# Kernel optimization log

Measured on AMD Instinct MI355X. Metric: run time of the kernel, lower is better.

The kernel has to match this reference:

```python
import jax, jax.numpy as jnp
import numpy as np
from jax.scipy.special import logsumexp

GROUP_LEN = 8
LABEL_SMOOTHING = 0.1
LOSS_TYPES = ("part_slice", "whole_slice", "part_block", "whole_block")
GN, D = 8192, 128


def setup_inputs() -> dict:
    key = jax.random.key(0)
    k1, k2 = jax.random.split(key)
    return {
        "image_features1": jax.random.normal(k1, (GN, D), dtype=jnp.float32),
        "image_features2": jax.random.normal(k2, (GN, D), dtype=jnp.float32),
        "logit_scale": jnp.float32(1.0 / 0.07),
    }


def _group_losses(S, G, N, eps):
    """Vectorized equivalents of the four Python-loop losses on an [GN,GN] logit matrix."""
    GN_ = G * N
    S4 = S.reshape(G, N, G, N)                      # [g, n, g2, n2]
    idx = jnp.arange(G)
    diag_blocks = S4[idx, :, idx, :]                # [G, N, N] (same-group blocks)

    # row-wise quantities
    row_lse = logsumexp(S, axis=1).reshape(G, N)    # [G, N]
    row_sum = S.sum(axis=1).reshape(G, N)           # [G, N]
    pos_sum = diag_blocks.sum(axis=-1)              # [G, N] sum over same-group cols

    # part_slice: mean_i (1-eps)(lse_i - pos_sum_i) + eps/(GN)(lse_i - row_sum_i)
    part_slice = jnp.mean((1.0 - eps) * (row_lse - pos_sum)
                          + (eps / GN_) * (row_lse - row_sum))

    # whole_slice: pos vector is row * y_i -> same-group entries plus (GN-N) zeros,
    # so lse(pos) = logaddexp(lse(diag entries), log(GN - N)) (exp(0)=1 per zero).
    diag_row_lse = logsumexp(diag_blocks, axis=-1)  # [G, N]
    pos_lse = jnp.logaddexp(diag_row_lse, jnp.log(jnp.float32(GN_ - N)))
    blk_row_lse = logsumexp(S4, axis=3)             # [G, N, G] per-row per-block lse
    ws_smooth = (row_lse[:, :, None] - blk_row_lse).sum(axis=-1)  # [G, N]
    whole_slice = jnp.mean((1.0 - eps) * (row_lse - pos_lse) + (eps / G) * ws_smooth)

    # group-level quantities
    grp_lse = logsumexp(S4, axis=(1, 2, 3))         # [G] lse over group's full row band
    grp_sum = S4.sum(axis=(1, 2, 3))                # [G]
    diag_sum = diag_blocks.sum(axis=(1, 2))         # [G]

    # part_block
    part_block = jnp.mean((1.0 - eps) * (grp_lse - diag_sum / (N * N))
                          + eps * (grp_lse - grp_sum / (G * N * N)))

    # whole_block
    blk_lse = logsumexp(S4, axis=(1, 3))            # [G, G] per block lse
    diag_blk_lse = blk_lse[idx, idx]                # [G]
    wb_smooth = (grp_lse[:, None] - blk_lse).sum(axis=-1)  # [G]
    whole_block = jnp.mean((1.0 - eps) * (grp_lse - diag_blk_lse) + (eps / G) * wb_smooth)

    return {"part_slice": part_slice, "whole_slice": whole_slice,
            "part_block": part_block, "whole_block": whole_block}


def reference(image_features1, image_features2, logit_scale):
    f1 = image_features1 / jnp.linalg.norm(image_features1, axis=-1, keepdims=True)
    f2 = image_features2 / jnp.linalg.norm(image_features2, axis=-1, keepdims=True)
    GN_, _ = f1.shape
    N = GROUP_LEN
    G = GN_ // N
    S1 = logit_scale * (f1 @ f2.T)                  # logits_per_image1 [GN, GN]
    S2 = S1.T                                       # logits_per_image2
    eps = LABEL_SMOOTHING
    l1 = _group_losses(S1, G, N, eps)
    l2 = _group_losses(S2, G, N, eps)
    loss = jnp.float32(0.0)
    for lt in LOSS_TYPES:
        loss = loss + 0.5 * (l1[lt] + l2[lt])
    return loss / len(LOSS_TYPES)
```

## Files before the change

kernel.cpp:

```cpp
#include <hip/hip_runtime.h>
#include <math.h>

typedef __attribute__((ext_vector_type(8))) short bf16x8;
typedef __attribute__((ext_vector_type(4))) float f32x4;
typedef unsigned short ushort_t;

#define GN 8192
#define NGRP 1024
#define DDIM 128
#define NCH 16
#define LOG2E 1.4426950408889634f
#define LN2 0.6931471805599453f

#if __has_builtin(__builtin_amdgcn_exp2f)
#define EXP2F(x) __builtin_amdgcn_exp2f(x)
#else
#define EXP2F(x) exp2f(x)
#endif
#if __has_builtin(__builtin_amdgcn_logf)
#define LOG2FAST(x) __builtin_amdgcn_logf(x)
#else
#define LOG2FAST(x) log2f(x)
#endif

#define ROWST 0
#define GRPB  (ROWST + GN*NCH*2)
#define DT    (GRPB + NGRP*NCH)
#define DU8   (DT + 2*GN)
#define GSUM  (DU8 + NGRP)
#define CSUMP (GSUM + 2*NGRP*DDIM)
#define COLP  (CSUMP + 2*32*DDIM)
#define GRP2P (COLP + 128*GN*2)
#define FIN2  (GRP2P + 128*NGRP)
#define SB2   (FIN2 + GN*2)
#define PART  (SB2 + NGRP)

__device__ __forceinline__ ushort_t f2bf(float x) {
  unsigned u = __float_as_uint(x);
  unsigned r = (u + 0x7fffu + ((u >> 16) & 1u)) >> 16;
  return (ushort_t)r;
}
__device__ __forceinline__ float bf2f(unsigned h) {
  return __uint_as_float(h << 16);
}

__device__ __forceinline__ float dpp_shr1_add(float v) {
  int s = __builtin_amdgcn_update_dpp(0, __float_as_int(v), 0x111, 0xF, 0xF, true);
  return v + __int_as_float(s);
}
__device__ __forceinline__ float dpp_shr2_add(float v) {
  int s = __builtin_amdgcn_update_dpp(0, __float_as_int(v), 0x112, 0xF, 0xF, true);
  return v + __int_as_float(s);
}
__device__ __forceinline__ float dpp_shr4_add(float v) {
  int s = __builtin_amdgcn_update_dpp(0, __float_as_int(v), 0x114, 0xF, 0xF, true);
  return v + __int_as_float(s);
}
__device__ __forceinline__ float dpp_ror8_add(float v) {
  int s = __builtin_amdgcn_update_dpp(0, __float_as_int(v), 0x128, 0xF, 0xF, true);
  return v + __int_as_float(s);
}

__global__ __launch_bounds__(256) void normg_kernel(
    const float* __restrict__ f1, const float* __restrict__ f2,
    const float* __restrict__ scp, ushort_t* __restrict__ wsu,
    float* __restrict__ wf) {
  const int b = blockIdx.x;
  const int m = b >> 10;
  const int g = b & 1023;
  const int t = threadIdx.x;
  const int r = t >> 5;
  const int c4 = t & 31;
  const float* __restrict__ f = m ? f2 : f1;
  const float fac0 = m ? 1.0f : (scp[0] * LOG2E);

  const float4 v = ((const float4*)(f + ((size_t)(g * 8 + r)) * DDIM))[c4];
  float ss = v.x * v.x + v.y * v.y + v.z * v.z + v.w * v.w;
  #pragma unroll
  for (int d = 1; d < 32; d <<= 1) ss += __shfl_xor(ss, d);
  const float inv = fac0 / sqrtf(ss);

  ushort4 o;
  o.x = f2bf(v.x * inv); o.y = f2bf(v.y * inv);
  o.z = f2bf(v.z * inv); o.w = f2bf(v.w * inv);
  ((ushort4*)(wsu + (size_t)m * GN * DDIM + (size_t)(g * 8 + r) * DDIM))[c4] = o;

  __shared__ float lds[8][DDIM];
  lds[r][c4 * 4 + 0] = bf2f(o.x);
  lds[r][c4 * 4 + 1] = bf2f(o.y);
  lds[r][c4 * 4 + 2] = bf2f(o.z);
  lds[r][c4 * 4 + 3] = bf2f(o.w);
  __syncthreads();
  if (t < DDIM) {
    float s = 0.f;
    #pragma unroll
    for (int j = 0; j < 8; ++j) s += lds[j][t];
    wf[GSUM + ((size_t)m * NGRP + g) * DDIM + t] = s;
  }
}

__global__ __launch_bounds__(128) void csum_kernel(float* __restrict__ wf) {
  const int b = blockIdx.x;
  const int m = b >> 5;
  const int seg = b & 31;
  const int k = threadIdx.x;
  const float* gp = wf + GSUM + ((size_t)m * NGRP + seg * 32) * DDIM + k;
  float s = 0.f;
  #pragma unroll 8
  for (int g = 0; g < 32; ++g) s += gp[(size_t)g * DDIM];
  wf[CSUMP + ((size_t)m * 32 + seg) * DDIM + k] = s;
}

__global__ __launch_bounds__(256, 4) void gemm_stats(
    const ushort_t* __restrict__ wsu, const float* __restrict__ scp,
    float* __restrict__ wf) {
  const int idx = blockIdx.x;
  const int rowblk = idx >> 4;
  const int chunk = idx & 15;
  const int t = threadIdx.x;
  const int w = t >> 6;
  const int l = t & 63;
  const int li = l & 15;
  const int q = l >> 4;
  const float C = scp[0];
  const float nC2 = -C * LOG2E;

  const ushort_t* A = wsu;
  const ushort_t* B = wsu + (size_t)GN * DDIM;
  const int row0 = rowblk * 64;

  __shared__ ushort_t As[64 * 128];
  {
    const int arow = t >> 2;
    const int aq = t & 3;
    const ushort_t* Agp = A + (size_t)(row0 + arow) * DDIM + aq * 32;
    #pragma unroll
    for (int j = 0; j < 4; ++j) {
      const int swz = (aq * 4 + j) ^ (arow & 15);
      *(uint4*)(As + arow * 128 + swz * 8) = *(const uint4*)(const void*)(Agp + j * 8);
    }
  }
  __syncthreads();

  float esum[4] = {0.f, 0.f, 0.f, 0.f};
  float sbl[4]  = {0.f, 0.f, 0.f, 0.f};
  float sBr[4]  = {0.f, 0.f, 0.f, 0.f};

  const ushort_t* Bp = B + ((size_t)(chunk * 512 + w * 16) + li) * DDIM + q * 8;
  const bool hasdia = (chunk == (row0 >> 9));
  const int idiag = (row0 & 511) >> 6;
  const f32x4 cinit = {nC2, nC2, nC2, nC2};

  #pragma unroll 1
  for (int i = 0; i < 8; ++i) {
    const ushort_t* Bi = Bp + (size_t)i * (64 * DDIM);
    bf16x8 bc[4];
    #pragma unroll
    for (int ks = 0; ks < 4; ++ks)
      bc[ks] = *(const bf16x8*)(const void*)(Bi + ks * 32);

    f32x4 acc[4];
    #pragma unroll
    for (int s = 0; s < 4; ++s) acc[s] = cinit;
    #pragma unroll
    for (int ks = 0; ks < 4; ++ks) {
      int co = (((ks * 4 + q) ^ li) * 8);
      asm volatile("" : "+v"(co));
      bf16x8 a0[4];
      #pragma unroll
      for (int s = 0; s < 4; ++s)
        a0[s] = *(const bf16x8*)(As + (16 * s + li) * 128 + co);
      #pragma unroll
      for (int s = 0; s < 4; ++s)
        acc[s] = __builtin_amdgcn_mfma_f32_16x16x32_bf16(bc[ks], a0[s], acc[s], 0, 0, 0);
    }

    const bool dia = hasdia && (i == idiag);
    const int cb = chunk * 512 + i * 64 + w * 16;
    float lvc = 0.f;
    float ecolp[4] = {0.f, 0.f, 0.f, 0.f};
    float prodc[4] = {1.f, 1.f, 1.f, 1.f};

    #pragma unroll
    for (int s = 0; s < 4; ++s) {
      float e[4];
      #pragma unroll
      for (int r = 0; r < 4; ++r) e[r] = EXP2F(acc[s][r]);
      float tt = (e[0] + e[1]) + (e[2] + e[3]);
      esum[s] += tt;
      float u = tt + __shfl_xor(tt, 16);
      sbl[s] += LOG2FAST(u);
      float bs = dpp_shr4_add(dpp_shr2_add(dpp_shr1_add(u)));
      float lg = LOG2FAST(bs);
      sBr[s] += lg;
      lvc += lg;

      #pragma unroll
      for (int r = 0; r < 4; ++r) {
        float o_ = dpp_shr4_add(dpp_shr2_add(dpp_shr1_add(e[r])));
        prodc[r] *= o_;
        ecolp[r] += o_;
        if (dia && w == s && ((li == 7 && q < 2) || (li == 15 && q >= 2)))
          wf[DT + GN + cb + q * 4 + r] = o_;
      }
      if (dia && w == s) {
        if (((q >> 1) == (li >> 3)) && ((q & 1) == 0))
          wf[DT + row0 + 16 * w + li] = u;
        if (l == 7)  wf[DU8 + rowblk * 8 + 2 * w]     = bs;
        if (l == 47) wf[DU8 + rowblk * 8 + 2 * w + 1] = bs;
      }
    }

    float lc[4];
    #pragma unroll
    for (int r = 0; r < 4; ++r) {
      ecolp[r] = dpp_ror8_add(ecolp[r]);
      lc[r] = LOG2FAST(prodc[r]);
      lc[r] = dpp_ror8_add(lc[r]);
    }
    lvc = dpp_ror8_add(lvc);
    if (li == 7) {
      #pragma unroll
      for (int r = 0; r < 4; ++r) {
        float2 st; st.x = ecolp[r]; st.y = lc[r];
        *(float2*)(wf + COLP + ((size_t)rowblk * GN + cb + q * 4 + r) * 2) = st;
      }
    }
    if (l == 7)  wf[GRP2P + (size_t)rowblk * NGRP + (cb >> 3)]     = lvc;
    if (l == 39) wf[GRP2P + (size_t)rowblk * NGRP + (cb >> 3) + 1] = lvc;
  }

  #pragma unroll
  for (int s = 0; s < 4; ++s) {
    esum[s] += __shfl_xor(esum[s], 16); esum[s] += __shfl_xor(esum[s], 32);
    sbl[s]  += __shfl_xor(sbl[s], 16);  sbl[s]  += __shfl_xor(sbl[s], 32);
    sBr[s]  += __shfl_xor(sBr[s], 16);  sBr[s]  += __shfl_xor(sBr[s], 32);
  }

  __shared__ float redE[4][64], redL[4][64], redB[4][8];
  if (q == 0) {
    #pragma unroll
    for (int s = 0; s < 4; ++s) {
      redE[w][16 * s + li] = esum[s];
      redL[w][16 * s + li] = 0.5f * sbl[s];
    }
  }
  if (l == 7) {
    #pragma unroll
    for (int s = 0; s < 4; ++s) redB[w][2 * s] = 0.5f * sBr[s];
  }
  if (l == 15) {
    #pragma unroll
    for (int s = 0; s < 4; ++s) redB[w][2 * s + 1] = 0.5f * sBr[s];
  }
  __syncthreads();

  if (t < 64) {
    const float E = redE[0][t] + redE[1][t] + redE[2][t] + redE[3][t];
    const float L = redL[0][t] + redL[1][t] + redL[2][t] + redL[3][t];
    const size_t o = ROWST + ((size_t)(row0 + t) * NCH + chunk) * 2;
    wf[o + 0] = E; wf[o + 1] = L;
  }
  if (t < 8) {
    const float s4 = redB[0][t] + redB[1][t] + redB[2][t] + redB[3][t];
    wf[GRPB + (size_t)(rowblk * 8 + t) * NCH + chunk] = s4;
  }
}

__global__ __launch_bounds__(256) void colred_kernel(float* __restrict__ wf) {
  const int b = blockIdx.x;
  const int t = threadIdx.x;
  const int lane = t & 31;
  const int slice = t >> 5;
  __shared__ float red[8][32][2];
  if (b < 256) {
    const int c = b * 32 + lane;
    float e = 0.f, ls = 0.f;
    #pragma unroll 4
    for (int k = 0; k < 16; ++k) {
      const int rb = slice * 16 + k;
      float2 v = *(const float2*)(wf + COLP + ((size_t)rb * GN + c) * 2);
      e += v.x; ls += v.y;
    }
    red[slice][lane][0] = e; red[slice][lane][1] = ls;
    __syncthreads();
    if (slice == 0) {
      float E = 0.f, L = 0.f;
      #pragma unroll
      for (int s2 = 0; s2 < 8; ++s2) { E += red[s2][lane][0]; L += red[s2][lane][1]; }
      wf[FIN2 + c * 2] = E; wf[FIN2 + c * 2 + 1] = L;
    }
  } else {
    const int cg = (b - 256) * 32 + lane;
    float s = 0.f;
    #pragma unroll 4
    for (int k = 0; k < 16; ++k) s += wf[GRP2P + (size_t)(slice * 16 + k) * NGRP + cg];
    red[slice][lane][0] = s;
    __syncthreads();
    if (slice == 0) {
      float S = 0.f;
      #pragma unroll
      for (int s2 = 0; s2 < 8; ++s2) S += red[s2][lane][0];
      wf[SB2 + cg] = S;
    }
  }
}

__global__ __launch_bounds__(256) void loss_kernel(
    const float* __restrict__ wf, const ushort_t* __restrict__ wsu,
    const float* __restrict__ scp, float* __restrict__ partials) {
  const int b = blockIdx.x;
  const int pass = b >> 5;
  const int rbase = (b & 31) * 256;
  const int t = threadIdx.x;
  const int row = rbase + t;
  const int g = row >> 3;
  const float C = scp[0];
  const float eps = 0.1f;

  __shared__ float cs_l[DDIM];
  if (t < DDIM) {
    const float* cp = wf + CSUMP + ((size_t)(pass ^ 1) * 32) * DDIM + t;
    float s = 0.f;
    #pragma unroll 8
    for (int seg = 0; seg < 32; ++seg) s += cp[(size_t)seg * DDIM];
    cs_l[t] = s;
  }
  __syncthreads();

  float E, L;
  if (pass == 0) {
    const size_t ro = ROWST + ((size_t)row * NCH) * 2;
    E = 0.f; L = 0.f;
    #pragma unroll
    for (int ch = 0; ch < NCH; ++ch) {
      E += wf[ro + 2 * ch];
      L += wf[ro + 2 * ch + 1];
    }
  } else {
    E = wf[FIN2 + row * 2];
    L = wf[FIN2 + row * 2 + 1];
  }

  const ushort_t* M = wsu + (size_t)pass * GN * DDIM + (size_t)row * DDIM;
  const float* gs = wf + GSUM + ((size_t)(pass ^ 1) * NGRP + g) * DDIM;
  float r2 = 0.f, p2 = 0.f;
  const uint4* Mv = (const uint4*)(const void*)M;
  #pragma unroll
  for (int c = 0; c < 8; ++c) {
    uint4 vv = Mv[c];
    unsigned uu[4] = {vv.x, vv.y, vv.z, vv.w};
    #pragma unroll
    for (int j = 0; j < 4; ++j) {
      float flo = bf2f(uu[j] & 0xffffu);
      float fhi = bf2f(uu[j] >> 16);
      const int k = c * 8 + j * 2;
      r2 += flo * cs_l[k];   r2 += fhi * cs_l[k + 1];
      p2 += flo * gs[k];     p2 += fhi * gs[k + 1];
    }
  }
  const float R = LN2 * r2;
  const float P = LN2 * p2;

  const float Td = wf[DT + (size_t)pass * GN + row];
  const float logE = __logf(E);
  const float row_lse = C + logE;

  float acc = ((1.f - eps) * (row_lse - P) + (eps / 8192.f) * (row_lse - R)) * (1.f / 8192.f);
  const float dl = C + __logf(Td);
  const float l8 = 9.0099363f;
  const float mx = fmaxf(dl, l8);
  const float pos_lse = mx + __logf(__expf(dl - mx) + __expf(l8 - mx));
  acc += ((1.f - eps) * (row_lse - pos_lse) + (eps / 1024.f) * (1024.f * logE - LN2 * L)) * (1.f / 8192.f);

  __shared__ float shE[256], shR[256], shP[256];
  shE[t] = E; shR[t] = R; shP[t] = P;
  __syncthreads();
  if (t < 32) {
    float Eg = 0.f, Rg = 0.f, Pg = 0.f;
    #pragma unroll
    for (int j = 0; j < 8; ++j) { Eg += shE[t * 8 + j]; Rg += shR[t * 8 + j]; Pg += shP[t * 8 + j]; }
    const int g2 = (rbase >> 3) + t;
    float SB;
    if (pass == 0) {
      SB = 0.f;
      #pragma unroll
      for (int ch = 0; ch < NCH; ++ch) SB += wf[GRPB + (size_t)g2 * NCH + ch];
    } else {
      SB = wf[SB2 + g2];
    }
    const float U = wf[DU8 + g2];
    const float logEg = __logf(Eg);
    const float grp_lse = C + logEg;
    acc += ((1.f - eps) * (grp_lse - Pg * (1.f / 64.f)) + eps * (grp_lse - Rg * (1.f / 65536.f))) * (1.f / 1024.f);
    const float dbl = C + __logf(U);
    acc += ((1.f - eps) * (grp_lse - dbl) + (eps / 1024.f) * (1024.f * logEg - LN2 * SB)) * (1.f / 1024.f);
  }

  #pragma unroll
  for (int d = 1; d < 64; d <<= 1) acc += __shfl_xor(acc, d);
  __shared__ float sr[4];
  if ((t & 63) == 0) sr[t >> 6] = acc;
  __syncthreads();
  if (t == 0) partials[b] = sr[0] + sr[1] + sr[2] + sr[3];
}

__global__ __launch_bounds__(64) void final_kernel(
    const float* __restrict__ partials, float* __restrict__ out) {
  const int t = threadIdx.x;
  float v = partials[t];
  #pragma unroll
  for (int d = 1; d < 64; d <<= 1) v += __shfl_xor(v, d);
  if (t == 0) out[0] = 0.125f * v;
}

extern "C" void kernel_launch(void* const* d_in, const int* in_sizes, int n_in,
                              void* d_out, int out_size, void* d_ws, size_t ws_size,
                              hipStream_t stream) {
  const float* f1 = (const float*)d_in[0];
  const float* f2 = (const float*)d_in[1];
  const float* sc = (const float*)d_in[2];
  ushort_t* wsu = (ushort_t*)d_ws;
  float* wf = (float*)((char*)d_ws + (size_t)2 * GN * DDIM * sizeof(ushort_t));
  float* out = (float*)d_out;

  hipLaunchKernelGGL(normg_kernel, dim3(2048), dim3(256), 0, stream, f1, f2, sc, wsu, wf);
  hipLaunchKernelGGL(csum_kernel, dim3(64), dim3(128), 0, stream, wf);
  hipLaunchKernelGGL(gemm_stats, dim3(2048), dim3(256), 0, stream, wsu, sc, wf);
  hipLaunchKernelGGL(colred_kernel, dim3(288), dim3(256), 0, stream, wf);
  hipLaunchKernelGGL(loss_kernel, dim3(64), dim3(256), 0, stream, wf, wsu, sc, wf + PART);
  hipLaunchKernelGGL(final_kernel, dim3(1), dim3(64), 0, stream, wf + PART, out);
}
```

Measured before the change: 68.14 us.

## Fold csum and final reduction kernels into neighbors to cut launch count

Removes the standalone csum kernel by adding 64 extra blocks to colred_kernel that compute the per-segment group column sums. It also removes final_kernel by having loss_kernel atomically accumulate its scaled partials into the output, which normg_kernel now zeroes. Separately, it rescales the column product accumulation by 2^24 per factor and subtracts 96 after the log, to avoid underflow in the product. Launch overhead drops from six kernels to four, in exchange for a nondeterministic float atomic sum order.

```diff
diff --git a/kernel.cpp b/kernel.cpp
--- a/kernel.cpp
+++ b/kernel.cpp
@@ -33,7 +33,6 @@
 #define GRP2P (COLP + 128*GN*2)
 #define FIN2  (GRP2P + 128*NGRP)
 #define SB2   (FIN2 + GN*2)
-#define PART  (SB2 + NGRP)
 
 __device__ __forceinline__ ushort_t f2bf(float x) {
   unsigned u = __float_as_uint(x);
@@ -64,11 +63,12 @@
 __global__ __launch_bounds__(256) void normg_kernel(
     const float* __restrict__ f1, const float* __restrict__ f2,
     const float* __restrict__ scp, ushort_t* __restrict__ wsu,
-    float* __restrict__ wf) {
+    float* __restrict__ wf, float* __restrict__ out) {
   const int b = blockIdx.x;
   const int m = b >> 10;
   const int g = b & 1023;
   const int t = threadIdx.x;
+  if (b == 0 && t == 0) out[0] = 0.f;
   const int r = t >> 5;
   const int c4 = t & 31;
   const float* __restrict__ f = m ? f2 : f1;
@@ -97,18 +97,6 @@
     for (int j = 0; j < 8; ++j) s += lds[j][t];
     wf[GSUM + ((size_t)m * NGRP + g) * DDIM + t] = s;
   }
-}
-
-__global__ __launch_bounds__(128) void csum_kernel(float* __restrict__ wf) {
-  const int b = blockIdx.x;
-  const int m = b >> 5;
-  const int seg = b & 31;
-  const int k = threadIdx.x;
-  const float* gp = wf + GSUM + ((size_t)m * NGRP + seg * 32) * DDIM + k;
-  float s = 0.f;
-  #pragma unroll 8
-  for (int g = 0; g < 32; ++g) s += gp[(size_t)g * DDIM];
-  wf[CSUMP + ((size_t)m * 32 + seg) * DDIM + k] = s;
 }
 
 __global__ __launch_bounds__(256, 4) void gemm_stats(
@@ -198,7 +186,7 @@
       #pragma unroll
       for (int r = 0; r < 4; ++r) {
         float o_ = dpp_shr4_add(dpp_shr2_add(dpp_shr1_add(e[r])));
-        prodc[r] *= o_;
+        prodc[r] *= o_ * 16777216.f;
         ecolp[r] += o_;
         if (dia && w == s && ((li == 7 && q < 2) || (li == 15 && q >= 2)))
           wf[DT + GN + cb + q * 4 + r] = o_;
@@ -215,7 +203,7 @@
     #pragma unroll
     for (int r = 0; r < 4; ++r) {
       ecolp[r] = dpp_ror8_add(ecolp[r]);
-      lc[r] = LOG2FAST(prodc[r]);
+      lc[r] = LOG2FAST(prodc[r]) - 96.f;
       lc[r] = dpp_ror8_add(lc[r]);
     }
     lvc = dpp_ror8_add(lvc);
@@ -290,7 +278,7 @@
       for (int s2 = 0; s2 < 8; ++s2) { E += red[s2][lane][0]; L += red[s2][lane][1]; }
       wf[FIN2 + c * 2] = E; wf[FIN2 + c * 2 + 1] = L;
     }
-  } else {
+  } else if (b < 288) {
     const int cg = (b - 256) * 32 + lane;
     float s = 0.f;
     #pragma unroll 4
@@ -303,12 +291,23 @@
       for (int s2 = 0; s2 < 8; ++s2) S += red[s2][lane][0];
       wf[SB2 + cg] = S;
     }
+  } else {
+    const int b2 = b - 288;
+    const int m = b2 >> 5;
+    const int seg = b2 & 31;
+    if (t < DDIM) {
+      const float* gp = wf + GSUM + ((size_t)m * NGRP + seg * 32) * DDIM + t;
+      float s = 0.f;
+      #pragma unroll 8
+      for (int g = 0; g < 32; ++g) s += gp[(size_t)g * DDIM];
+      wf[CSUMP + ((size_t)m * 32 + seg) * DDIM + t] = s;
+    }
   }
 }
 
 __global__ __launch_bounds__(256) void loss_kernel(
     const float* __restrict__ wf, const ushort_t* __restrict__ wsu,
-    const float* __restrict__ scp, float* __restrict__ partials) {
+    const float* __restrict__ scp, float* __restrict__ out) {
   const int b = blockIdx.x;
   const int pass = b >> 5;
   const int rbase = (b & 31) * 256;
@@ -402,16 +401,7 @@
   __shared__ float sr[4];
   if ((t & 63) == 0) sr[t >> 6] = acc;
   __syncthreads();
-  if (t == 0) partials[b] = sr[0] + sr[1] + sr[2] + sr[3];
-}
-
-__global__ __launch_bounds__(64) void final_kernel(
-    const float* __restrict__ partials, float* __restrict__ out) {
-  const int t = threadIdx.x;
-  float v = partials[t];
-  #pragma unroll
-  for (int d = 1; d < 64; d <<= 1) v += __shfl_xor(v, d);
-  if (t == 0) out[0] = 0.125f * v;
+  if (t == 0) atomicAdd(out, 0.125f * (sr[0] + sr[1] + sr[2] + sr[3]));
 }
 
 extern "C" void kernel_launch(void* const* d_in, const int* in_sizes, int n_in,
@@ -424,10 +414,8 @@
   float* wf = (float*)((char*)d_ws + (size_t)2 * GN * DDIM * sizeof(ushort_t));
   float* out = (float*)d_out;
 
-  hipLaunchKernelGGL(normg_kernel, dim3(2048), dim3(256), 0, stream, f1, f2, sc, wsu, wf);
-  hipLaunchKernelGGL(csum_kernel, dim3(64), dim3(128), 0, stream, wf);
+  hipLaunchKernelGGL(normg_kernel, dim3(2048), dim3(256), 0, stream, f1, f2, sc, wsu, wf, out);
   hipLaunchKernelGGL(gemm_stats, dim3(2048), dim3(256), 0, stream, wsu, sc, wf);
-  hipLaunchKernelGGL(colred_kernel, dim3(288), dim3(256), 0, stream, wf);
-  hipLaunchKernelGGL(loss_kernel, dim3(64), dim3(256), 0, stream, wf, wsu, sc, wf + PART);
-  hipLaunchKernelGGL(final_kernel, dim3(1), dim3(64), 0, stream, wf + PART, out);
-}
+  hipLaunchKernelGGL(colred_kernel, dim3(352), dim3(256), 0, stream, wf);
+  hipLaunchKernelGGL(loss_kernel, dim3(64), dim3(256), 0, stream, wf, wsu, sc, out);
+}
```

Result: faster. 64.61 us (median of 2 runs) (-5.2%).
